# Kernel tuning notes

Hardware: AMD Instinct MI355X
Metric: run time of the kernel (lower is better)

## Reference

```python
import jax, jax.numpy as jnp
import numpy as np

HEAD_DIM = 128
N_HEADS = 32
N_KV_HEADS = 8
ROPE_BASE = 500000.0
QK_EPS = 1e-6


def _rope_cos_sin(position_ids, head_dim, base, dtype):
    # position_ids: [B, S] int -> cos/sin [B, 1, S, head_dim]
    inv_freq = 1.0 / (base ** (jnp.arange(0, head_dim, 2, dtype=jnp.float32) / head_dim))
    freqs = position_ids.astype(jnp.float32)[..., None] * inv_freq  # [B, S, D/2]
    emb = jnp.concatenate([freqs, freqs], axis=-1)  # [B, S, D]
    return jnp.cos(emb).astype(dtype)[:, None], jnp.sin(emb).astype(dtype)[:, None]


def _rotate_half(x):
    x1, x2 = jnp.split(x, 2, axis=-1)
    return jnp.concatenate([-x2, x1], axis=-1)


def _qk_norm(x, scale, eps):
    # L2 norm (not RMS): scale * x / (||x||_2 + eps)
    norm = jnp.sqrt(jnp.sum(x * x, axis=-1, keepdims=True))
    return scale * x / (norm + eps)


def setup_inputs() -> dict:
    key = jax.random.key(0)
    ks = jax.random.split(key, 7)
    B, S, H = 1, 2048, 4096
    kv_dim = N_KV_HEADS * HEAD_DIM
    return {
        "hidden_states": jax.random.normal(ks[0], (B, S, H), dtype=jnp.float32),
        "position_ids": jnp.broadcast_to(jnp.arange(S, dtype=jnp.int64 if jax.config.jax_enable_x64 else jnp.int32), (B, S)),
        "Wq": jax.random.normal(ks[1], (H, H), dtype=jnp.float32) * (H ** -0.5),
        "Wk": jax.random.normal(ks[2], (kv_dim, H), dtype=jnp.float32) * (H ** -0.5),
        "Wv": jax.random.normal(ks[3], (kv_dim, H), dtype=jnp.float32) * (H ** -0.5),
        "Wo": jax.random.normal(ks[4], (H, H), dtype=jnp.float32) * (H ** -0.5),
        "q_scale": jnp.ones((HEAD_DIM,), dtype=jnp.float32),
        "k_scale": jnp.ones((HEAD_DIM,), dtype=jnp.float32),
    }


def reference(hidden_states, position_ids, Wq, Wk, Wv, Wo, q_scale, k_scale):
    B, S, H = hidden_states.shape
    scaling = 1.0 / np.sqrt(HEAD_DIM)

    # projections (torch Linear: y = x @ W.T)
    q = (hidden_states @ Wq.T).reshape(B, S, N_HEADS, HEAD_DIM).transpose(0, 2, 1, 3)
    k = (hidden_states @ Wk.T).reshape(B, S, N_KV_HEADS, HEAD_DIM).transpose(0, 2, 1, 3)
    v = (hidden_states @ Wv.T).reshape(B, S, N_KV_HEADS, HEAD_DIM).transpose(0, 2, 1, 3)

    cos, sin = _rope_cos_sin(position_ids, HEAD_DIM, ROPE_BASE, q.dtype)
    q = q * cos + _rotate_half(q) * sin
    k = k * cos + _rotate_half(k) * sin

    q = _qk_norm(q, q_scale, QK_EPS)
    k = _qk_norm(k, k_scale, QK_EPS)

    # GQA: repeat kv heads to match query heads
    n_rep = N_HEADS // N_KV_HEADS
    k = jnp.repeat(k, n_rep, axis=1)  # [B, n_heads, S, D]
    v = jnp.repeat(v, n_rep, axis=1)

    # causal SDPA
    scores = jnp.einsum("bhqd,bhkd->bhqk", q, k) * scaling
    causal = jnp.tril(jnp.ones((S, S), dtype=bool))
    scores = jnp.where(causal, scores, jnp.finfo(scores.dtype).min)
    attn = jax.nn.softmax(scores, axis=-1)
    out = jnp.einsum("bhqk,bhkd->bhqd", attn, v)  # [B, H, S, D]

    out = out.transpose(0, 2, 1, 3).reshape(B, S, H)
    return out @ Wo.T
```

## Files before the change

kernel.cpp:

```cpp
#include <hip/hip_runtime.h>
#include <math.h>

typedef unsigned short u16;
typedef unsigned int u32;
typedef __attribute__((ext_vector_type(8))) short bf16x8;
typedef __attribute__((ext_vector_type(4))) float f32x4;

#define S_LEN 2048
#define HID 4096
#define NH 32
#define NKV 8
#define HD 128
#define QS 6144

__device__ __forceinline__ u16 f2bf(float f) {
  u32 u = __float_as_uint(f);
  u32 r = (u + 0x7FFFu + ((u >> 16) & 1u)) >> 16;
  return (u16)r;
}
__device__ __forceinline__ float bf2f(u16 v) {
  return __uint_as_float(((u32)v) << 16);
}
__device__ __forceinline__ f32x4 mfma16(bf16x8 a, bf16x8 b, f32x4 c) {
  return __builtin_amdgcn_mfma_f32_16x16x32_bf16(a, b, c, 0, 0, 0);
}
__device__ __forceinline__ void async16(const u16* g, u16* l) {
  __builtin_amdgcn_global_load_lds(
      (__attribute__((address_space(1))) void*)g,
      (__attribute__((address_space(3))) void*)l, 16, 0, 0);
}
#if __has_builtin(__builtin_amdgcn_exp2f)
#define EXP2(x) __builtin_amdgcn_exp2f(x)
#else
#define EXP2(x) exp2f(x)
#endif

#define VMC(n) asm volatile("s_waitcnt vmcnt(" #n ")" ::: "memory")
#define BAR __builtin_amdgcn_s_barrier()

__global__ __launch_bounds__(256) void conv_all(
    const float* __restrict__ hs, const float* __restrict__ wq,
    const float* __restrict__ wk, const float* __restrict__ wv,
    const float* __restrict__ wo, u16* __restrict__ dhs, u16* __restrict__ dwq,
    u16* __restrict__ dwk, u16* __restrict__ dwv, u16* __restrict__ dwo) {
  int i = blockIdx.x * 256 + threadIdx.x;
  const float* src;
  u16* dst;
  int off;
  if (i < 2097152) { src = hs; dst = dhs; off = 0; }
  else if (i < 6291456) { src = wq; dst = dwq; off = 2097152; }
  else if (i < 7340032) { src = wk; dst = dwk; off = 6291456; }
  else if (i < 8388608) { src = wv; dst = dwv; off = 7340032; }
  else { src = wo; dst = dwo; off = 8388608; }
  int j = i - off;
  float4 v = ((const float4*)src)[j];
  ushort4 o;
  o.x = f2bf(v.x); o.y = f2bf(v.y); o.z = f2bf(v.z); o.w = f2bf(v.w);
  ((ushort4*)dst)[j] = o;
}


#define DSA(dst, qi, d)                                                    \
  {                                                                        \
    const u16* p_ = As + (d)*16384 + (wm * 64 + (qi)*32 + cl) * 64;        \
    _Pragma("unroll") for (int ii = 0; ii < 2; ii++)                       \
        _Pragma("unroll") for (int kk = 0; kk < 2; kk++)                   \
            dst[ii][kk] =                                                  \
        *(const bf16x8*)(p_ + ii * 1024 + ((c0 ^ (kk << 2)) << 3));        \
  }

#define DSB(dst, qj, d)                                                    \
  {                                                                        \
    const u16* p_ =                                                        \
        Bs + (d)*BSTR + (wn * (BN / 2) + (qj) * (BN / 4) + cl) * 64;       \
    _Pragma("unroll") for (int jj = 0; jj < NJ; jj++)                      \
        _Pragma("unroll") for (int kk = 0; kk < 2; kk++)                   \
            dst[jj][kk] =                                                  \
        *(const bf16x8*)(p_ + jj * 1024 + ((c0 ^ (kk << 2)) << 3));        \
  }

#define MM(qi, qj, asrc, bsrc)                                             \
  {                                                                        \
    _Pragma("unroll") for (int kk = 0; kk < 2; kk++)                       \
        _Pragma("unroll") for (int ii = 0; ii < 2; ii++)                   \
            _Pragma("unroll") for (int jj = 0; jj < NJ; jj++)              \
                acc[(qi)*2 + ii][(qj)*NJ + jj] =                           \
        mfma16(asrc[ii][kk], bsrc[jj][kk], acc[(qi)*2 + ii][(qj)*NJ + jj]);\
  }

#define PH2(MMA1, MMA2)                                          \
  {                                                              \
    BAR;                                                         \
    MMA1; MMA2;                                                  \
    BAR;                                                         \
  }

template <int NJ>
__global__ __launch_bounds__(512, 2) void gemm4p(
    const u16* __restrict__ A, const u16* __restrict__ B,
    u16* __restrict__ Cb, float* __restrict__ Cf, int N, int K) {
  constexpr int BN = NJ * 64;
  constexpr int BSTR = BN * 64;
  extern __shared__ u16 lds[];
  u16* As = lds;
  u16* Bs = lds + 32768;
  const int tid = threadIdx.x;
  const int lane = tid & 63, wv = tid >> 6;
  const int cl = lane & 15, qd = lane >> 4;
  const int wm = wv >> 1, wn = wv & 1;
  const int c0 = qd ^ (cl & 7);

  const int cpx = gridDim.x >> 3;
  const int swz = (blockIdx.x & 7) * cpx + (blockIdx.x >> 3);
  const int m0 = (swz & 7) * 256;
  const int n0 = (swz >> 3) * BN;

  u32 aof[4], bof[NJ];
#pragma unroll
  for (int q = 0; q < 4; q++) {
    int r = q * 64 + wv * 8 + (lane >> 3);
    int c = (lane & 7) ^ (r & 7);
    aof[q] = (u32)(m0 + r) * K + c * 8;
  }
#pragma unroll
  for (int q = 0; q < NJ; q++) {
    int r = q * 64 + wv * 8 + (lane >> 3);
    int c = (lane & 7) ^ (r & 7);
    bof[q] = (u32)(n0 + r) * K + c * 8;
  }
  const int sbo = wv * 512;

  auto STAll = [&](int tt, int d) {
#pragma unroll
    for (int q = 0; q < 4; q++)
      async16(A + (size_t)tt * 64 + aof[q], As + d * 16384 + q * 4096 + sbo);
  };
  auto STBall = [&](int tt, int d) {
#pragma unroll
    for (int q = 0; q < NJ; q++)
      async16(B + (size_t)tt * 64 + bof[q], Bs + d * BSTR + q * 4096 + sbo);
  };

  f32x4 acc[4][2 * NJ];
  f32x4 zz = {0.f, 0.f, 0.f, 0.f};
#pragma unroll
  for (int i = 0; i < 4; i++)
#pragma unroll
    for (int j = 0; j < 2 * NJ; j++) acc[i][j] = zz;
  bf16x8 A0r[2][2], A1r[2][2], B0r[NJ][2], B1r[NJ][2];

  const int NT = K >> 6;

  STAll(0, 0); STBall(0, 0); STAll(1, 1);
  VMC(4);
  BAR;

  for (int it = 0; it < (NT >> 1); ++it) {
    const int t = it * 2;
    const bool s2 = (t + 2) < NT;
    DSA(A0r, 0, 0); DSA(A1r, 1, 0); DSB(B0r, 0, 0);
    STBall(t + 1, 1);
    PH2(MM(0, 0, A0r, B0r), MM(1, 0, A1r, B0r));
    DSB(B1r, 1, 0);
    if (s2) {
      STAll(t + 2, 0);
      VMC(4);
    } else {
      VMC(0);
    }
    PH2(MM(0, 1, A0r, B1r), MM(1, 1, A1r, B1r));
    DSA(A0r, 0, 1); DSA(A1r, 1, 1); DSB(B0r, 0, 1);
    if (s2) STBall(t + 2, 0);
    PH2(MM(0, 0, A0r, B0r), MM(1, 0, A1r, B0r));
    DSB(B1r, 1, 1);
    if (s2) {
      STAll(t + 3, 1);
      VMC(4);
    } else {
      VMC(0);
    }
    PH2(MM(0, 1, A0r, B1r), MM(1, 1, A1r, B1r));
  }

#pragma unroll
  for (int i = 0; i < 4; i++)
#pragma unroll
    for (int j = 0; j < 2 * NJ; j++) {
      int row = m0 + wm * 64 + i * 16 + qd * 4;
      int col = n0 + wn * (BN / 2) + (j / NJ) * (BN / 4) + (j % NJ) * 16 + cl;
#pragma unroll
      for (int r = 0; r < 4; r++) {
        float v = acc[i][j][r];
        if (Cb) Cb[(size_t)(row + r) * N + col] = f2bf(v);
        else    Cf[(size_t)(row + r) * N + col] = v;
      }
    }
}

__global__ __launch_bounds__(256) void rope_l2norm(
    u16* __restrict__ x, const int* __restrict__ pos_ids,
    const float* __restrict__ scale, int hmask, int hshift, int stride) {
  const int lane = threadIdx.x & 63;
  const int wv = threadIdx.x >> 6;
  const int idx = blockIdx.x * 4 + wv;
  const int s = idx >> hshift;
  const int h = idx & hmask;
  u16* p = x + (size_t)s * stride + h * HD;
  const float pos = (float)pos_ids[s];
  const float inv = expf((float)lane * -0.20503692777194264f);
  float sn, cs;
  sincosf(pos * inv, &sn, &cs);
  float a = bf2f(p[lane]);
  float b = bf2f(p[lane + 64]);
  float ra = a * cs - b * sn;
  float rb = b * cs + a * sn;
  float ss = ra * ra + rb * rb;
#pragma unroll
  for (int off = 32; off >= 1; off >>= 1) ss += __shfl_xor(ss, off, 64);
  float rd = 1.0f / (sqrtf(ss) + 1e-6f);
  p[lane] = f2bf(scale[lane] * ra * rd);
  p[lane + 64] = f2bf(scale[lane + 64] * rb * rd);
}

__global__ __launch_bounds__(256) void transpose_v(const u16* __restrict__ v,
                                                   u16* __restrict__ vt) {
  __shared__ u16 t[64][65];
  const int r = threadIdx.x >> 6;
  const int c = threadIdx.x & 63;
  const int s0 = blockIdx.x * 64, d0 = blockIdx.y * 64;
#pragma unroll
  for (int i = 0; i < 16; i++) {
    int row = i * 4 + r;
    t[row][c] = v[(size_t)(s0 + row) * QS + d0 + c];
  }
  __syncthreads();
#pragma unroll
  for (int i = 0; i < 16; i++) {
    int row = i * 4 + r;
    vt[(size_t)(d0 + row) * S_LEN + s0 + c] = t[c][row];
  }
}

#define PLD 68

__global__ __launch_bounds__(512) void flash_attn(
    const u16* __restrict__ QKV, const u16* __restrict__ Vt,
    u16* __restrict__ O) {
  extern __shared__ u16 alds[];
  u16* Ks = alds;
  u16* Vs = alds + 16384;
  u16* Ps = alds + 32768;
  const int tid = threadIdx.x;
  const int lane = tid & 63, wv = tid >> 6;
  const int cl = lane & 15, qd = lane >> 4;
  const int h = blockIdx.y;
  const int kvh = h >> 2;
  const float es = 0.12751629240081506f;

  const u16* Kbase = QKV + 4096 + kvh * HD;
  const u16* Vbase = Vt + (size_t)kvh * HD * S_LEN;

  auto stage = [&](int kt, int d) {
#pragma unroll
    for (int q = 0; q < 2; q++) {
      int c = q * 512 + wv * 64 + lane;
      int kr = c >> 4, kg = (c & 15) ^ (kr & 15);
      async16(Kbase + (size_t)(kt * 64 + kr) * QS + kg * 8,
              Ks + d * 8192 + (q * 512 + wv * 64) * 8);
      int vr = c >> 3, vg = (c & 7) ^ (vr & 7);
      async16(Vbase + (size_t)vr * S_LEN + kt * 64 + vg * 8,
              Vs + d * 8192 + (q * 512 + wv * 64) * 8);
    }
  };

  for (int half = 0; half < 2; half++) {
    const int qbi = half ? (15 - (int)blockIdx.x) : (int)blockIdx.x;
    const int q0 = qbi * 128;

    bf16x8 aQ[4];
    {
      const u16* qrow =
          QKV + (size_t)(q0 + wv * 16 + cl) * QS + h * HD + qd * 8;
#pragma unroll
      for (int kk = 0; kk < 4; kk++) aQ[kk] = *(const bf16x8*)(qrow + kk * 32);
    }

    f32x4 oacc[8];
    f32x4 zz = {0.f, 0.f, 0.f, 0.f};
#pragma unroll
    for (int n = 0; n < 8; n++) oacc[n] = zz;
    float lsum[4] = {0.f, 0.f, 0.f, 0.f};

    const int row_min = q0 + wv * 16;
    const int ktmax = 2 * qbi + 1;

    int cur = 0;
    stage(0, 0);
    for (int kt = 0; kt <= ktmax; kt++) {
      if (kt < ktmax) stage(kt + 1, cur ^ 1);
      if (kt == 0) {
        VMC(4);
        BAR;
      }
      const int koff = cur * 8192;

      if (kt * 64 <= row_min + 15) {
        f32x4 sacc[4];
#pragma unroll
        for (int j = 0; j < 4; j++) sacc[j] = zz;
#pragma unroll
        for (int kk = 0; kk < 4; kk++) {
#pragma unroll
          for (int j = 0; j < 4; j++) {
            int row = j * 16 + cl;
            int ch = (kk * 4 + qd) ^ (row & 15);
            bf16x8 bK = *(const bf16x8*)&Ks[koff + row * 128 + ch * 8];
            sacc[j] = mfma16(aQ[kk], bK, sacc[j]);
          }
        }

        float pm[4][4];
        if (kt * 64 + 63 > row_min) {
          const int grow = row_min + qd * 4;
#pragma unroll
          for (int j = 0; j < 4; j++) {
            int gcol = kt * 64 + j * 16 + cl;
#pragma unroll
            for (int r = 0; r < 4; r++)
              pm[j][r] = (gcol <= grow + r) ? EXP2(sacc[j][r] * es) : 0.f;
          }
        } else {
#pragma unroll
          for (int j = 0; j < 4; j++)
#pragma unroll
            for (int r = 0; r < 4; r++) pm[j][r] = EXP2(sacc[j][r] * es);
        }
#pragma unroll
        for (int j = 0; j < 4; j++)
#pragma unroll
          for (int r = 0; r < 4; r++) lsum[r] += pm[j][r];

#pragma unroll
        for (int j = 0; j < 4; j++)
#pragma unroll
          for (int r = 0; r < 4; r++)
            Ps[(wv * 16 + qd * 4 + r) * PLD + j * 16 + cl] = f2bf(pm[j][r]);
        __asm__ volatile("s_waitcnt lgkmcnt(0)" ::: "memory");

#pragma unroll
        for (int kk = 0; kk < 2; kk++) {
          bf16x8 aP =
              *(const bf16x8*)&Ps[(wv * 16 + cl) * PLD + kk * 32 + qd * 8];
#pragma unroll
          for (int n = 0; n < 8; n++) {
            int row = n * 16 + cl;
            int ch = (kk * 4 + qd) ^ (row & 7);
            bf16x8 bV = *(const bf16x8*)&Vs[koff + row * 64 + ch * 8];
            oacc[n] = mfma16(aP, bV, oacc[n]);
          }
        }
      }

      VMC(0);
      BAR;
      cur ^= 1;
    }

#pragma unroll
    for (int r = 0; r < 4; r++) {
#pragma unroll
      for (int off = 8; off >= 1; off >>= 1)
        lsum[r] += __shfl_xor(lsum[r], off, 64);
    }
#pragma unroll
    for (int r = 0; r < 4; r++) {
      float il = 1.0f / lsum[r];
      int row = row_min + qd * 4 + r;
#pragma unroll
      for (int n = 0; n < 8; n++)
        O[(size_t)row * HID + h * HD + n * 16 + cl] = f2bf(oacc[n][r] * il);
    }
  }
}

extern "C" void kernel_launch(void* const* d_in, const int* in_sizes, int n_in,
                              void* d_out, int out_size, void* d_ws, size_t ws_size,
                              hipStream_t stream) {
  const float* hs = (const float*)d_in[0];
  const int* pos = (const int*)d_in[1];
  const float* Wq = (const float*)d_in[2];
  const float* Wk = (const float*)d_in[3];
  const float* Wv = (const float*)d_in[4];
  const float* Wo = (const float*)d_in[5];
  const float* qsc = (const float*)d_in[6];
  const float* ksc = (const float*)d_in[7];
  float* out = (float*)d_out;
  char* ws = (char*)d_ws;
  const size_t MB = 1u << 20;

  u16* hs_b  = (u16*)(ws + 0 * MB);
  u16* wq_b  = (u16*)(ws + 16 * MB);
  u16* wk_b  = (u16*)(ws + 48 * MB);
  u16* wv_b  = (u16*)(ws + 56 * MB);
  u16* qkv_b = (u16*)(ws + 64 * MB);
  u16* vt_b  = (u16*)(ws + 88 * MB);
  u16* wo_b  = (u16*)(ws + 92 * MB);
  u16* o_b   = hs_b;

  static bool attr_set = false;
  if (!attr_set) {
    hipFuncSetAttribute(reinterpret_cast<const void*>(&gemm4p<3>),
                        hipFuncAttributeMaxDynamicSharedMemorySize, 114688);
    hipFuncSetAttribute(reinterpret_cast<const void*>(&gemm4p<2>),
                        hipFuncAttributeMaxDynamicSharedMemorySize, 98304);
    hipFuncSetAttribute(reinterpret_cast<const void*>(&flash_attn),
                        hipFuncAttributeMaxDynamicSharedMemorySize, 82944);
    attr_set = true;
  }

  conv_all<<<49152, 256, 0, stream>>>(hs, Wq, Wk, Wv, Wo,
                                      hs_b, wq_b, wk_b, wv_b, wo_b);

  gemm4p<3><<<dim3(8 * (QS / 192)), 512, 114688, stream>>>(
      hs_b, wq_b, qkv_b, nullptr, QS, HID);

  rope_l2norm<<<S_LEN * NH / 4, 256, 0, stream>>>(qkv_b, pos, qsc, NH - 1, 5, QS);
  rope_l2norm<<<S_LEN * NKV / 4, 256, 0, stream>>>(qkv_b + 4096, pos, ksc, NKV - 1, 3, QS);
  transpose_v<<<dim3(S_LEN / 64, (NKV * HD) / 64), 256, 0, stream>>>(qkv_b + 5120, vt_b);

  flash_attn<<<dim3(8, NH), 512, 82944, stream>>>(qkv_b, vt_b, o_b);

  gemm4p<2><<<dim3(8 * (HID / 128)), 512, 98304, stream>>>(
      o_b, wo_b, nullptr, out, HID, HID);
}
```

Baseline: 448.9 us.

## Halve GEMM M-tile to 128 rows and regrid warps 2x4 for occupancy

Both projection GEMMs now use 128-row tiles instead of 256 and lay out the eight waves as 2x4 over M and N, with one K-slice of fragments loaded per MFMA phase. LDS per block drops and the launch bound asks for 4 blocks per CU, doubling the grid. The aim is more blocks in flight and fewer registers per wave. The cost is lower arithmetic intensity per block, more barriers per K-step, and more redundant global loads of B.

```diff
diff --git a/kernel.cpp b/kernel.cpp
--- a/kernel.cpp
+++ b/kernel.cpp
@@ -60,64 +60,52 @@
 }
 
 
-#define DSA(dst, qi, d)                                                    \
+#define DSA(d, kk)                                                         \
   {                                                                        \
-    const u16* p_ = As + (d)*16384 + (wm * 64 + (qi)*32 + cl) * 64;        \
-    _Pragma("unroll") for (int ii = 0; ii < 2; ii++)                       \
-        _Pragma("unroll") for (int kk = 0; kk < 2; kk++)                   \
-            dst[ii][kk] =                                                  \
-        *(const bf16x8*)(p_ + ii * 1024 + ((c0 ^ (kk << 2)) << 3));        \
-  }
-
-#define DSB(dst, qj, d)                                                    \
+    const u16* p_ = As + (d)*8192 + (wm * 64 + cl) * 64;                   \
+    _Pragma("unroll") for (int ii = 0; ii < 4; ii++)                       \
+        Ar[ii] = *(const bf16x8*)(p_ + ii * 1024 +                         \
+                                  ((c0 ^ ((kk) << 2)) << 3));              \
+  }
+
+#define DSB(d, kk)                                                         \
   {                                                                        \
-    const u16* p_ =                                                        \
-        Bs + (d)*BSTR + (wn * (BN / 2) + (qj) * (BN / 4) + cl) * 64;       \
+    const u16* p_ = Bs + (d)*BSTR + (wn * (BN / 4) + cl) * 64;             \
     _Pragma("unroll") for (int jj = 0; jj < NJ; jj++)                      \
-        _Pragma("unroll") for (int kk = 0; kk < 2; kk++)                   \
-            dst[jj][kk] =                                                  \
-        *(const bf16x8*)(p_ + jj * 1024 + ((c0 ^ (kk << 2)) << 3));        \
-  }
-
-#define MM(qi, qj, asrc, bsrc)                                             \
+        Br[jj] = *(const bf16x8*)(p_ + jj * 1024 +                         \
+                                  ((c0 ^ ((kk) << 2)) << 3));              \
+  }
+
+#define MMK()                                                              \
   {                                                                        \
-    _Pragma("unroll") for (int kk = 0; kk < 2; kk++)                       \
-        _Pragma("unroll") for (int ii = 0; ii < 2; ii++)                   \
-            _Pragma("unroll") for (int jj = 0; jj < NJ; jj++)              \
-                acc[(qi)*2 + ii][(qj)*NJ + jj] =                           \
-        mfma16(asrc[ii][kk], bsrc[jj][kk], acc[(qi)*2 + ii][(qj)*NJ + jj]);\
-  }
-
-#define PH2(MMA1, MMA2)                                          \
-  {                                                              \
-    BAR;                                                         \
-    MMA1; MMA2;                                                  \
-    BAR;                                                         \
+    _Pragma("unroll") for (int ii = 0; ii < 4; ii++)                       \
+        _Pragma("unroll") for (int jj = 0; jj < NJ; jj++)                  \
+            acc[ii][jj] = mfma16(Ar[ii], Br[jj], acc[ii][jj]);             \
   }
 
 template <int NJ>
-__global__ __launch_bounds__(512, 2) void gemm4p(
+__global__ __launch_bounds__(512, 4) void gemm4p(
     const u16* __restrict__ A, const u16* __restrict__ B,
     u16* __restrict__ Cb, float* __restrict__ Cf, int N, int K) {
   constexpr int BN = NJ * 64;
   constexpr int BSTR = BN * 64;
   extern __shared__ u16 lds[];
   u16* As = lds;
-  u16* Bs = lds + 32768;
+  u16* Bs = lds + 16384;
   const int tid = threadIdx.x;
   const int lane = tid & 63, wv = tid >> 6;
   const int cl = lane & 15, qd = lane >> 4;
-  const int wm = wv >> 1, wn = wv & 1;
+  const int wm = wv >> 2, wn = wv & 3;
   const int c0 = qd ^ (cl & 7);
 
   const int cpx = gridDim.x >> 3;
   const int swz = (blockIdx.x & 7) * cpx + (blockIdx.x >> 3);
-  const int m0 = (swz & 7) * 256;
-  const int n0 = (swz >> 3) * BN;
-
-  u32 aof[4], bof[NJ];
-#pragma unroll
-  for (int q = 0; q < 4; q++) {
+  const int m0 = (swz & 15) * 128;
+  const int n0 = (swz >> 4) * BN;
+
+  u32 aof[2], bof[NJ];
+#pragma unroll
+  for (int q = 0; q < 2; q++) {
     int r = q * 64 + wv * 8 + (lane >> 3);
     int c = (lane & 7) ^ (r & 7);
     aof[q] = (u32)(m0 + r) * K + c * 8;
@@ -132,8 +120,8 @@
 
   auto STAll = [&](int tt, int d) {
 #pragma unroll
-    for (int q = 0; q < 4; q++)
-      async16(A + (size_t)tt * 64 + aof[q], As + d * 16384 + q * 4096 + sbo);
+    for (int q = 0; q < 2; q++)
+      async16(A + (size_t)tt * 64 + aof[q], As + d * 8192 + q * 4096 + sbo);
   };
   auto STBall = [&](int tt, int d) {
 #pragma unroll
@@ -141,53 +129,53 @@
       async16(B + (size_t)tt * 64 + bof[q], Bs + d * BSTR + q * 4096 + sbo);
   };
 
-  f32x4 acc[4][2 * NJ];
+  f32x4 acc[4][NJ];
   f32x4 zz = {0.f, 0.f, 0.f, 0.f};
 #pragma unroll
   for (int i = 0; i < 4; i++)
 #pragma unroll
-    for (int j = 0; j < 2 * NJ; j++) acc[i][j] = zz;
-  bf16x8 A0r[2][2], A1r[2][2], B0r[NJ][2], B1r[NJ][2];
+    for (int j = 0; j < NJ; j++) acc[i][j] = zz;
+  bf16x8 Ar[4], Br[NJ];
 
   const int NT = K >> 6;
 
   STAll(0, 0); STBall(0, 0); STAll(1, 1);
-  VMC(4);
+  VMC(2);
   BAR;
 
   for (int it = 0; it < (NT >> 1); ++it) {
     const int t = it * 2;
     const bool s2 = (t + 2) < NT;
-    DSA(A0r, 0, 0); DSA(A1r, 1, 0); DSB(B0r, 0, 0);
+    DSA(0, 0); DSB(0, 0);
     STBall(t + 1, 1);
-    PH2(MM(0, 0, A0r, B0r), MM(1, 0, A1r, B0r));
-    DSB(B1r, 1, 0);
+    BAR; MMK(); BAR;
+    DSA(0, 1); DSB(0, 1);
     if (s2) {
       STAll(t + 2, 0);
-      VMC(4);
+      VMC(2);
     } else {
       VMC(0);
     }
-    PH2(MM(0, 1, A0r, B1r), MM(1, 1, A1r, B1r));
-    DSA(A0r, 0, 1); DSA(A1r, 1, 1); DSB(B0r, 0, 1);
+    BAR; MMK(); BAR;
+    DSA(1, 0); DSB(1, 0);
     if (s2) STBall(t + 2, 0);
-    PH2(MM(0, 0, A0r, B0r), MM(1, 0, A1r, B0r));
-    DSB(B1r, 1, 1);
+    BAR; MMK(); BAR;
+    DSA(1, 1); DSB(1, 1);
     if (s2) {
       STAll(t + 3, 1);
-      VMC(4);
+      VMC(2);
     } else {
       VMC(0);
     }
-    PH2(MM(0, 1, A0r, B1r), MM(1, 1, A1r, B1r));
+    BAR; MMK(); BAR;
   }
 
 #pragma unroll
   for (int i = 0; i < 4; i++)
 #pragma unroll
-    for (int j = 0; j < 2 * NJ; j++) {
+    for (int j = 0; j < NJ; j++) {
       int row = m0 + wm * 64 + i * 16 + qd * 4;
-      int col = n0 + wn * (BN / 2) + (j / NJ) * (BN / 4) + (j % NJ) * 16 + cl;
+      int col = n0 + wn * (BN / 4) + j * 16 + cl;
 #pragma unroll
       for (int r = 0; r < 4; r++) {
         float v = acc[i][j][r];
@@ -410,9 +398,9 @@
   static bool attr_set = false;
   if (!attr_set) {
     hipFuncSetAttribute(reinterpret_cast<const void*>(&gemm4p<3>),
-                        hipFuncAttributeMaxDynamicSharedMemorySize, 114688);
+                        hipFuncAttributeMaxDynamicSharedMemorySize, 81920);
     hipFuncSetAttribute(reinterpret_cast<const void*>(&gemm4p<2>),
-                        hipFuncAttributeMaxDynamicSharedMemorySize, 98304);
+                        hipFuncAttributeMaxDynamicSharedMemorySize, 65536);
     hipFuncSetAttribute(reinterpret_cast<const void*>(&flash_attn),
                         hipFuncAttributeMaxDynamicSharedMemorySize, 82944);
     attr_set = true;
@@ -421,7 +409,7 @@
   conv_all<<<49152, 256, 0, stream>>>(hs, Wq, Wk, Wv, Wo,
                                       hs_b, wq_b, wk_b, wv_b, wo_b);
 
-  gemm4p<3><<<dim3(8 * (QS / 192)), 512, 114688, stream>>>(
+  gemm4p<3><<<dim3(16 * (QS / 192)), 512, 81920, stream>>>(
       hs_b, wq_b, qkv_b, nullptr, QS, HID);
 
   rope_l2norm<<<S_LEN * NH / 4, 256, 0, stream>>>(qkv_b, pos, qsc, NH - 1, 5, QS);
@@ -430,6 +418,6 @@
 
   flash_attn<<<dim3(8, NH), 512, 82944, stream>>>(qkv_b, vt_b, o_b);
 
-  gemm4p<2><<<dim3(8 * (HID / 128)), 512, 98304, stream>>>(
+  gemm4p<2><<<dim3(16 * (HID / 128)), 512, 65536, stream>>>(
       o_b, wo_b, nullptr, out, HID, HID);
 }
```

Measured after the change: 496.9 us. 1.11x slower.

## Fuse fp32-to-bf16 weight conversion into GEMM B-tile loads

Applied to the files above, without the earlier changes.

Drops the separate conversion pass over Wq/Wk/Wv/Wo. The GEMMs now read fp32 weights straight from global memory into registers, convert them to bf16 and write them to swizzled LDS, with row selection picking among the three QKV weight matrices. This removes a full read/write pass over about 48M weights, but each GEMM block now reads fp32 weights (twice the bytes, reread by all 8 M-blocks) through register staging instead of async LDS loads, and the vmcnt waits had to be retuned.

```diff
diff --git a/kernel.cpp b/kernel.cpp
--- a/kernel.cpp
+++ b/kernel.cpp
@@ -37,26 +37,15 @@
 
 #define VMC(n) asm volatile("s_waitcnt vmcnt(" #n ")" ::: "memory")
 #define BAR __builtin_amdgcn_s_barrier()
-
-__global__ __launch_bounds__(256) void conv_all(
-    const float* __restrict__ hs, const float* __restrict__ wq,
-    const float* __restrict__ wk, const float* __restrict__ wv,
-    const float* __restrict__ wo, u16* __restrict__ dhs, u16* __restrict__ dwq,
-    u16* __restrict__ dwk, u16* __restrict__ dwv, u16* __restrict__ dwo) {
+#define CFENCE asm volatile("" ::: "memory")
+
+__global__ __launch_bounds__(256) void conv_hs(const float* __restrict__ hs,
+                                               u16* __restrict__ dst) {
   int i = blockIdx.x * 256 + threadIdx.x;
-  const float* src;
-  u16* dst;
-  int off;
-  if (i < 2097152) { src = hs; dst = dhs; off = 0; }
-  else if (i < 6291456) { src = wq; dst = dwq; off = 2097152; }
-  else if (i < 7340032) { src = wk; dst = dwk; off = 6291456; }
-  else if (i < 8388608) { src = wv; dst = dwv; off = 7340032; }
-  else { src = wo; dst = dwo; off = 8388608; }
-  int j = i - off;
-  float4 v = ((const float4*)src)[j];
+  float4 v = ((const float4*)hs)[i];
   ushort4 o;
   o.x = f2bf(v.x); o.y = f2bf(v.y); o.z = f2bf(v.z); o.w = f2bf(v.w);
-  ((ushort4*)dst)[j] = o;
+  ((ushort4*)dst)[i] = o;
 }
 
 
@@ -95,10 +84,18 @@
     BAR;                                                         \
   }
 
+#define VMCP2()                             \
+  do {                                      \
+    if constexpr (NJ == 3) VMC(10);         \
+    else VMC(8);                            \
+  } while (0)
+
 template <int NJ>
 __global__ __launch_bounds__(512, 2) void gemm4p(
-    const u16* __restrict__ A, const u16* __restrict__ B,
-    u16* __restrict__ Cb, float* __restrict__ Cf, int N, int K) {
+    const u16* __restrict__ A, const float* __restrict__ W0,
+    const float* __restrict__ W1, const float* __restrict__ W2,
+    int nb1, int nb2, u16* __restrict__ Cb, float* __restrict__ Cf,
+    int N, int K) {
   constexpr int BN = NJ * 64;
   constexpr int BSTR = BN * 64;
   extern __shared__ u16 lds[];
@@ -115,30 +112,54 @@
   const int m0 = (swz & 7) * 256;
   const int n0 = (swz >> 3) * BN;
 
-  u32 aof[4], bof[NJ];
+  u32 aof[4];
 #pragma unroll
   for (int q = 0; q < 4; q++) {
     int r = q * 64 + wv * 8 + (lane >> 3);
     int c = (lane & 7) ^ (r & 7);
     aof[q] = (u32)(m0 + r) * K + c * 8;
   }
-#pragma unroll
-  for (int q = 0; q < NJ; q++) {
-    int r = q * 64 + wv * 8 + (lane >> 3);
-    int c = (lane & 7) ^ (r & 7);
-    bof[q] = (u32)(n0 + r) * K + c * 8;
-  }
   const int sbo = wv * 512;
+
+  const float* bptr[2 * NJ];
+  u32 bwr[2 * NJ];
+#pragma unroll
+  for (int rq = 0; rq < 2 * NJ; rq++) {
+    int rl = rq * 32 + (tid >> 4);
+    int gc = tid & 15;
+    int row = n0 + rl;
+    const float* p = (row < nb1) ? (W0 + (size_t)row * K)
+                   : (row < nb2) ? (W1 + (size_t)(row - nb1) * K)
+                                 : (W2 + (size_t)(row - nb2) * K);
+    bptr[rq] = p + gc * 4;
+    bwr[rq] = (u32)rl * 64 + (((gc >> 1) ^ (rl & 7)) * 8) + ((gc & 1) * 4);
+  }
 
   auto STAll = [&](int tt, int d) {
 #pragma unroll
     for (int q = 0; q < 4; q++)
       async16(A + (size_t)tt * 64 + aof[q], As + d * 16384 + q * 4096 + sbo);
   };
-  auto STBall = [&](int tt, int d) {
-#pragma unroll
-    for (int q = 0; q < NJ; q++)
-      async16(B + (size_t)tt * 64 + bof[q], Bs + d * BSTR + q * 4096 + sbo);
+
+  float4 bv[2 * NJ];
+  auto ldB = [&]() {
+#pragma unroll
+    for (int rq = 0; rq < 2 * NJ; rq++) {
+      bv[rq] = *(const float4*)bptr[rq];
+      bptr[rq] += 64;
+    }
+  };
+  auto wrB = [&](int d) {
+#pragma unroll
+    for (int rq = 0; rq < 2 * NJ; rq++) {
+      u32 lo = (u32)f2bf(bv[rq].x) | ((u32)f2bf(bv[rq].y) << 16);
+      u32 hi = (u32)f2bf(bv[rq].z) | ((u32)f2bf(bv[rq].w) << 16);
+      uint2 wd;
+      wd.x = lo;
+      wd.y = hi;
+      *(uint2*)(Bs + d * BSTR + bwr[rq]) = wd;
+    }
+    CFENCE;
   };
 
   f32x4 acc[4][2 * NJ];
@@ -151,26 +172,32 @@
 
   const int NT = K >> 6;
 
-  STAll(0, 0); STBall(0, 0); STAll(1, 1);
+  STAll(0, 0);
+  STAll(1, 1);
+  ldB();
+  wrB(0);
   VMC(4);
+  asm volatile("s_waitcnt lgkmcnt(0)" ::: "memory");
   BAR;
 
   for (int it = 0; it < (NT >> 1); ++it) {
     const int t = it * 2;
     const bool s2 = (t + 2) < NT;
+    ldB();
     DSA(A0r, 0, 0); DSA(A1r, 1, 0); DSB(B0r, 0, 0);
-    STBall(t + 1, 1);
+    wrB(1);
     PH2(MM(0, 0, A0r, B0r), MM(1, 0, A1r, B0r));
     DSB(B1r, 1, 0);
     if (s2) {
+      ldB();
       STAll(t + 2, 0);
-      VMC(4);
+      VMCP2();
     } else {
       VMC(0);
     }
     PH2(MM(0, 1, A0r, B1r), MM(1, 1, A1r, B1r));
     DSA(A0r, 0, 1); DSA(A1r, 1, 1); DSB(B0r, 0, 1);
-    if (s2) STBall(t + 2, 0);
+    if (s2) wrB(0);
     PH2(MM(0, 0, A0r, B0r), MM(1, 0, A1r, B0r));
     DSB(B1r, 1, 1);
     if (s2) {
@@ -399,12 +426,8 @@
   const size_t MB = 1u << 20;
 
   u16* hs_b  = (u16*)(ws + 0 * MB);
-  u16* wq_b  = (u16*)(ws + 16 * MB);
-  u16* wk_b  = (u16*)(ws + 48 * MB);
-  u16* wv_b  = (u16*)(ws + 56 * MB);
   u16* qkv_b = (u16*)(ws + 64 * MB);
   u16* vt_b  = (u16*)(ws + 88 * MB);
-  u16* wo_b  = (u16*)(ws + 92 * MB);
   u16* o_b   = hs_b;
 
   static bool attr_set = false;
@@ -418,11 +441,10 @@
     attr_set = true;
   }
 
-  conv_all<<<49152, 256, 0, stream>>>(hs, Wq, Wk, Wv, Wo,
-                                      hs_b, wq_b, wk_b, wv_b, wo_b);
+  conv_hs<<<8192, 256, 0, stream>>>(hs, hs_b);
 
   gemm4p<3><<<dim3(8 * (QS / 192)), 512, 114688, stream>>>(
-      hs_b, wq_b, qkv_b, nullptr, QS, HID);
+      hs_b, Wq, Wk, Wv, 4096, 5120, qkv_b, nullptr, QS, HID);
 
   rope_l2norm<<<S_LEN * NH / 4, 256, 0, stream>>>(qkv_b, pos, qsc, NH - 1, 5, QS);
   rope_l2norm<<<S_LEN * NKV / 4, 256, 0, stream>>>(qkv_b + 4096, pos, ksc, NKV - 1, 3, QS);
@@ -431,5 +453,5 @@
   flash_attn<<<dim3(8, NH), 512, 82944, stream>>>(qkv_b, vt_b, o_b);
 
   gemm4p<2><<<dim3(8 * (HID / 128)), 512, 98304, stream>>>(
-      o_b, wo_b, nullptr, out, HID, HID);
-}
+      o_b, Wo, Wo, Wo, HID, HID, nullptr, out, HID, HID);
+}
```

Measured after the change: 523.6 us. +16.6%, slower.
